# Optimization experiments

Measured on AMD Instinct MI355X. Metric: run time of the kernel, lower is better.

Reference implementation:

```python
import jax, jax.numpy as jnp
import numpy as np

# PointLSTM (CVPR'20, VIPL-SLP repo) reference.
# Layout: inputs (B, C, T, N); first OFF channels of C are point coords (x,y,z,t).
# Per timestep t: for each point, find TOPK nearest (xyz) points of frame t-1,
# gather their positions / hidden / cell states, form [feat, pos_offset, h_nbr],
# apply a shared 1x1 conv producing 4*HID gates, LSTM-gate per neighbor, then
# max-pool over the TOPK neighbors. offsets arg is accepted but unused because
# PointLSTM is constructed with offsets=False (the wrapper's default).

B, C, T, N = 4, 132, 32, 64
HID, OFF, K = 256, 4, 16


def setup_inputs() -> dict:
    key = jax.random.key(0)
    k1, k2, k3 = jax.random.split(key, 3)
    inputs = jax.random.normal(k1, (B, C, T, N), jnp.float32)
    offsets = jax.random.normal(k2, (B, OFF, T, N), jnp.float32)
    cin = C + OFF + HID  # current feat + position offset + neighbor hidden
    W = jax.random.normal(k3, (4 * HID, cin), jnp.float32) / np.sqrt(cin)
    b = jnp.zeros((4 * HID,), jnp.float32)
    return {"inputs": inputs, "offsets": offsets, "W": W, "b": b}


def _gather(x, idx):
    # x: (B, C, N), idx: (B, N, K) -> (B, C, N, K)
    return jax.vmap(lambda xb, ib: xb[:, ib])(x, idx)


def _forward(inputs, offsets, W, b):
    pos = inputs[:, :OFF]               # (B, 4, T, N)
    xs = jnp.moveaxis(inputs, 2, 0)     # (T, B, C, N)
    ps = jnp.moveaxis(pos, 2, 0)        # (T, B, 4, N)
    h0 = jnp.zeros((B, HID, N), inputs.dtype)
    c0 = jnp.zeros((B, HID, N), inputs.dtype)

    def step(carry, xt_pt):
        h, c, prev_pos = carry          # h,c: (B,HID,N); prev_pos: (B,4,N)
        xt, pt = xt_pt                  # (B,C,N), (B,4,N)
        # squared xyz distance current frame -> previous frame: (B, N, N)
        d = jnp.sum((pt[:, :3, :, None] - prev_pos[:, :3, None, :]) ** 2, axis=1)
        _, idx = jax.lax.top_k(-d, K)   # (B, N, K) nearest neighbors
        pos_g = _gather(prev_pos, idx)  # (B, 4,  N, K)
        h_g = _gather(h, idx)           # (B, HID, N, K)
        c_g = _gather(c, idx)           # (B, HID, N, K)
        off = pos_g - pt[:, :, :, None]                      # position offsets
        xk = jnp.broadcast_to(xt[:, :, :, None], (B, C, N, K))
        comb = jnp.concatenate([xk, off, h_g], axis=1)       # (B, C+4+HID, N, K)
        gates = jnp.einsum('gc,bcnk->bgnk', W, comb) + b[None, :, None, None]
        i, f, o, g = jnp.split(gates, 4, axis=1)
        c_k = jax.nn.sigmoid(f) * c_g + jax.nn.sigmoid(i) * jnp.tanh(g)
        h_k = jax.nn.sigmoid(o) * jnp.tanh(c_k)
        h_new = jnp.max(h_k, axis=-1)   # AdaptiveMaxPool2d((None,1)) over K
        c_new = jnp.max(c_k, axis=-1)
        return (h_new, c_new, pt), (h_new, idx)

    # t=0 groups against its own frame with zero hidden state (repo behavior)
    _, (hs, idxs) = jax.lax.scan(step, (h0, c0, ps[0]), (xs, ps))
    out = jnp.moveaxis(hs, 0, 2)                         # (B, HID, T, N)
    inds = jnp.moveaxis(idxs, 0, 1).astype(jnp.int32)    # (B, T, N, K)
    return out, inds


def reference(inputs, offsets, W, b):
    # Matches TestPointLSTM.forward: (output[0][0].squeeze(-1), output[2])
    return _forward(inputs, offsets, W, b)
```

## Files before the change

kernel.cpp:

```cpp
#include <hip/hip_runtime.h>
#include <math.h>

#define BB 4
#define CC 132
#define TT 32
#define NN 64
#define HIDD 256
#define G4 1024
#define CIN 392
#define KK 16
#define HOFF 136

typedef __attribute__((ext_vector_type(8))) short bf16x8;
typedef __attribute__((ext_vector_type(4))) float f32x4;

__device__ __forceinline__ float frcp(float x) { return __builtin_amdgcn_rcpf(x); }
__device__ __forceinline__ float fsigm(float x) { return frcp(1.0f + __expf(-x)); }
__device__ __forceinline__ float ftanh(float x) {
    float e = __expf(2.0f * x);
    return 1.0f - 2.0f * frcp(e + 1.0f);
}
__device__ __forceinline__ unsigned short f2bf(float x) {
    union { float f; unsigned u; } v; v.f = x;
    unsigned r = v.u + 0x7fffu + ((v.u >> 16) & 1u);
    return (unsigned short)(r >> 16);
}

__global__ __launch_bounds__(256) void ktrans2(const float* __restrict__ W,
                                               const float* __restrict__ bias,
                                               unsigned short* __restrict__ WXf,
                                               unsigned short* __restrict__ WHf,
                                               unsigned short* __restrict__ WposA,
                                               float* __restrict__ biasP) {
    int gt = blockIdx.x;
    int tid = threadIdx.x;
    __shared__ float Wl[16][CIN];
    for (int row = 0; row < 16; ++row) {
        int orig = (row & 3) * 256 + gt * 4 + (row >> 2);
        for (int c = tid; c < CIN; c += 256)
            Wl[row][c] = W[(size_t)orig * CIN + c];
    }
    __syncthreads();
    for (int f = tid; f < 320; f += 256) {
        int ks = f >> 6, l = f & 63;
        bf16x8 v;
        #pragma unroll
        for (int j = 0; j < 8; ++j) {
            int c = ks * 32 + (l >> 4) * 8 + j;
            float w = (c < CC) ? Wl[l & 15][c] : ((c < HOFF) ? -Wl[l & 15][c] : 0.0f);
            v[j] = (short)f2bf(w);
        }
        *(bf16x8*)&WXf[((size_t)(gt * 5 + ks)) * 512 + l * 8] = v;
    }
    for (int f = tid; f < 512; f += 256) {
        int ks = f >> 6, l = f & 63;
        bf16x8 v;
        #pragma unroll
        for (int j = 0; j < 8; ++j) {
            int c = HOFF + ks * 32 + (l >> 4) * 8 + j;
            v[j] = (short)f2bf(Wl[l & 15][c]);
        }
        *(bf16x8*)&WHf[((size_t)(gt * 8 + ks)) * 512 + l * 8] = v;
    }
    if (tid < 64) {
        bf16x8 v;
        #pragma unroll
        for (int e = 0; e < 8; ++e) {
            int c = (tid >> 4) * 8 + e;
            v[e] = (c < 4) ? (short)f2bf(Wl[tid & 15][CC + c]) : (short)0;
        }
        *(bf16x8*)&WposA[(size_t)gt * 512 + tid * 8] = v;
    }
    if (tid < 16)
        biasP[gt * 16 + tid] = bias[(tid & 3) * 256 + gt * 4 + (tid >> 2)];
}

__global__ __launch_bounds__(256) void kprep(const float* __restrict__ in,
                                             int* __restrict__ idxw,
                                             float* __restrict__ outI,
                                             unsigned short* __restrict__ xf,
                                             unsigned short* __restrict__ posAf) {
    int t = blockIdx.x >> 2, b = blockIdx.x & 3;
    int tid = threadIdx.x;
    int tprev = t ? t - 1 : 0;

    __shared__ unsigned short X[64][160];
    {
        int n = tid & 63, cg = tid >> 6;
        for (int c = cg; c < 160; c += 4) {
            float v = 0.0f;
            if (c < CC)        v = in[(((size_t)b * CC + c) * TT + t) * NN + n];
            else if (c < HOFF) v = in[(((size_t)b * CC + (c - CC)) * TT + t) * NN + n];
            X[n][c] = f2bf(v);
        }
        __syncthreads();
        for (int i = 0; i < 5; ++i) {
            int f = i * 256 + tid;
            int mtn = f / 320, r = f % 320;
            int ks = r >> 6, l = r & 63;
            uint4 v = *(const uint4*)&X[mtn * 16 + (l & 15)][ks * 32 + (l >> 4) * 8];
            *(uint4*)&xf[(((size_t)(blockIdx.x * 4 + mtn)) * 5 + ks) * 512 + l * 8] = v;
        }
    }
    {
        int mt = tid >> 6, l = tid & 63;
        bf16x8 v;
        #pragma unroll
        for (int e = 0; e < 8; ++e) {
            int c = (l >> 4) * 8 + e;
            float p = (c < 4) ? in[(((size_t)b * CC + c) * TT + tprev) * NN + mt * 16 + (l & 15)] : 0.0f;
            v[e] = (short)f2bf(p);
        }
        *(bf16x8*)&posAf[(((size_t)(t * BB + b)) * 4 + mt) * 512 + l * 8] = v;
    }
    {
        int lane = tid & 63, w = tid >> 6;
        const float* base = in + (size_t)b * CC * TT * NN;
        float p0 = base[(0 * TT + tprev) * NN + lane];
        float p1 = base[(1 * TT + tprev) * NN + lane];
        float p2 = base[(2 * TT + tprev) * NN + lane];
        float q0 = base[(0 * TT + t) * NN + lane];
        float q1 = base[(1 * TT + t) * NN + lane];
        float q2 = base[(2 * TT + t) * NN + lane];
        for (int nn = 0; nn < 16; ++nn) {
            int n = w * 16 + nn;
            float a0 = __shfl(q0, n), a1 = __shfl(q1, n), a2 = __shfl(q2, n);
            float dx = a0 - p0, dy = a1 - p1, dz = a2 - p2;
            float s01 = __fadd_rn(__fmul_rn(dx, dx), __fmul_rn(dy, dy));
            float d = __fadd_rn(s01, __fmul_rn(dz, dz));
            unsigned long long key =
                ((unsigned long long)__float_as_uint(d) << 32) | (unsigned)lane;
            #pragma unroll
            for (int k = 2; k <= 64; k <<= 1) {
                #pragma unroll
                for (int j = k >> 1; j > 0; j >>= 1) {
                    unsigned long long other = __shfl_xor(key, j);
                    bool up = (lane & k) == 0;
                    bool upper = (lane & j) != 0;
                    bool keepMax = up ? upper : !upper;
                    unsigned long long mn = key < other ? key : other;
                    unsigned long long mx = key < other ? other : key;
                    key = keepMax ? mx : mn;
                }
            }
            if (lane < KK) {
                int m = (int)(key & 0xffffffffu);
                idxw[((t * BB + b) * NN + n) * KK + lane] = m;
                outI[((b * TT + t) * NN + n) * KK + lane] = (float)m;
            }
        }
    }
}

__global__ __launch_bounds__(256) void kxa3(const unsigned short* __restrict__ xf,
                                            const unsigned short* __restrict__ WXf,
                                            const float* __restrict__ biasP,
                                            float* __restrict__ XA) {
    int gq = blockIdx.x & 3, tb = blockIdx.x >> 2;
    int w = threadIdx.x >> 6, l = threadIdx.x & 63;
    int gbase = gq * 16 + w * 4;
    f32x4 acc[4][4];
    #pragma unroll
    for (int a = 0; a < 4; ++a)
        #pragma unroll
        for (int g = 0; g < 4; ++g) acc[a][g] = (f32x4){0.f, 0.f, 0.f, 0.f};
    #pragma unroll
    for (int ks = 0; ks < 5; ++ks) {
        bf16x8 af[4], bfr[4];
        #pragma unroll
        for (int m = 0; m < 4; ++m)
            af[m] = *(const bf16x8*)&xf[(((size_t)(tb * 4 + m)) * 5 + ks) * 512 + l * 8];
        #pragma unroll
        for (int g = 0; g < 4; ++g)
            bfr[g] = *(const bf16x8*)&WXf[((size_t)((gbase + g) * 5 + ks)) * 512 + l * 8];
        #pragma unroll
        for (int m = 0; m < 4; ++m)
            #pragma unroll
            for (int g = 0; g < 4; ++g)
                acc[m][g] = __builtin_amdgcn_mfma_f32_16x16x32_bf16(af[m], bfr[g], acc[m][g], 0, 0, 0);
    }
    int rb = tb * 64;
    #pragma unroll
    for (int g = 0; g < 4; ++g) {
        int gcol = (gbase + g) * 16 + (l & 15);
        float bv = biasP[gcol];
        #pragma unroll
        for (int m = 0; m < 4; ++m)
            #pragma unroll
            for (int r = 0; r < 4; ++r) {
                int row = rb + m * 16 + (l >> 4) * 4 + r;
                XA[(size_t)row * G4 + gcol] = acc[m][g][r] + bv;
            }
    }
}

__global__ __launch_bounds__(512) void kstep(const float* __restrict__ XA,
                                             const unsigned short* __restrict__ WHf,
                                             const unsigned short* __restrict__ WposA,
                                             const unsigned short* __restrict__ posAf,
                                             const unsigned short* __restrict__ hr,
                                             unsigned short* __restrict__ hw,
                                             const int* __restrict__ idxw,
                                             const float* __restrict__ cp,
                                             float* __restrict__ cn,
                                             float* __restrict__ out, int t) {
    int bid = blockIdx.x;
    int b = bid & 3, q = (bid >> 2) & 15, nh = bid >> 6;
    int tid = threadIdx.x;
    __shared__ float LDSG[64][68];
    __shared__ float cmbH[256], cmbC[256];

    int kh = tid >> 8, p = tid & 255;
    int nl = p >> 4, jl = p & 15;
    int n = nh * 16 + nl;
    int jg = q * 16 + jl;

    const int* irow = &idxw[((size_t)(t * BB + b) * NN + n) * KK + kh * 8];
    int4 mi0 = *(const int4*)irow;
    int4 mi1 = *(const int4*)(irow + 4);
    const float4 xav = *(const float4*)&XA[((size_t)(t * BB + b) * NN + n) * G4 + jg * 4];

    {
        int wv = tid >> 6, l = tid & 63;
        int mt = wv & 3, gh = wv >> 2;
        bf16x8 bf[8];
        if (t > 0) {
            #pragma unroll
            for (int ks = 0; ks < 8; ++ks)
                bf[ks] = *(const bf16x8*)&hr[(((size_t)(b * 4 + mt)) * 8 + ks) * 512 + l * 8];
        }
        bf16x8 bp = *(const bf16x8*)&posAf[(((size_t)(t * BB + b)) * 4 + mt) * 512 + l * 8];
        #pragma unroll
        for (int gg = 0; gg < 2; ++gg) {
            int gtl = gh * 2 + gg;
            int gt = q * 4 + gtl;
            f32x4 a0 = {0.f, 0.f, 0.f, 0.f};
            f32x4 a1 = {0.f, 0.f, 0.f, 0.f};
            if (t > 0) {
                #pragma unroll
                for (int ks = 0; ks < 8; ks += 2) {
                    bf16x8 af0 = *(const bf16x8*)&WHf[(((size_t)gt) * 8 + ks) * 512 + l * 8];
                    bf16x8 af1 = *(const bf16x8*)&WHf[(((size_t)gt) * 8 + ks + 1) * 512 + l * 8];
                    a0 = __builtin_amdgcn_mfma_f32_16x16x32_bf16(af0, bf[ks], a0, 0, 0, 0);
                    a1 = __builtin_amdgcn_mfma_f32_16x16x32_bf16(af1, bf[ks + 1], a1, 0, 0, 0);
                }
            }
            bf16x8 ap = *(const bf16x8*)&WposA[(size_t)gt * 512 + l * 8];
            a0 = __builtin_amdgcn_mfma_f32_16x16x32_bf16(ap, bp, a0, 0, 0, 0);
            a0[0] += a1[0]; a0[1] += a1[1]; a0[2] += a1[2]; a0[3] += a1[3];
            *(f32x4*)&LDSG[mt * 16 + (l & 15)][gtl * 16 + (l >> 4) * 4] = a0;
        }
    }

    float cgv[8] = {0.f, 0.f, 0.f, 0.f, 0.f, 0.f, 0.f, 0.f};
    if (t > 0) {
        const float* cb = cp + (size_t)b * NN * HIDD + jg;
        cgv[0] = cb[(size_t)mi0.x * HIDD];
        cgv[1] = cb[(size_t)mi0.y * HIDD];
        cgv[2] = cb[(size_t)mi0.z * HIDD];
        cgv[3] = cb[(size_t)mi0.w * HIDD];
        cgv[4] = cb[(size_t)mi1.x * HIDD];
        cgv[5] = cb[(size_t)mi1.y * HIDD];
        cgv[6] = cb[(size_t)mi1.z * HIDD];
        cgv[7] = cb[(size_t)mi1.w * HIDD];
    }
    __syncthreads();

    {
        int ms[8] = {mi0.x, mi0.y, mi0.z, mi0.w, mi1.x, mi1.y, mi1.z, mi1.w};
        float hmax = -INFINITY, cmax = -INFINITY;
        #pragma unroll
        for (int kk = 0; kk < 8; ++kk) {
            int m = ms[kk];
            f32x4 g = *(const f32x4*)&LDSG[m][jl * 4];
            float gi = xav.x + g[0];
            float gf = xav.y + g[1];
            float go = xav.z + g[2];
            float gg = xav.w + g[3];
            float ck = fsigm(gf) * cgv[kk] + fsigm(gi) * ftanh(gg);
            float hk = fsigm(go) * ftanh(ck);
            hmax = fmaxf(hmax, hk);
            cmax = fmaxf(cmax, ck);
        }
        if (kh == 1) { cmbH[p] = hmax; cmbC[p] = cmax; }
        __syncthreads();
        if (kh == 0) {
            hmax = fmaxf(hmax, cmbH[p]);
            cmax = fmaxf(cmax, cmbC[p]);
            cn[((size_t)b * NN + n) * HIDD + jg] = cmax;
            out[((size_t)(b * HIDD + jg) * TT + t) * NN + n] = hmax;
            hw[(((size_t)(b * 4 + (n >> 4))) * 8 + (jg >> 5)) * 512 +
               (((jg >> 3) & 3) * 16 + (n & 15)) * 8 + (jg & 7)] = f2bf(hmax);
        }
    }
}

extern "C" void kernel_launch(void* const* d_in, const int* in_sizes, int n_in,
                              void* d_out, int out_size, void* d_ws, size_t ws_size,
                              hipStream_t stream) {
    const float* in   = (const float*)d_in[0];
    const float* W    = (const float*)d_in[2];
    const float* bias = (const float*)d_in[3];
    float* out  = (float*)d_out;
    float* outI = out + (size_t)BB * HIDD * TT * NN;

    float* ws     = (float*)d_ws;
    float* XA     = ws;
    float* biasP  = XA + (size_t)TT * BB * NN * G4;
    float* c0     = biasP + G4;
    float* c1     = c0 + (size_t)BB * NN * HIDD;
    unsigned short* WXf   = (unsigned short*)(c1 + (size_t)BB * NN * HIDD);
    unsigned short* WHf   = WXf + (size_t)64 * 5 * 512;
    unsigned short* WposA = WHf + (size_t)64 * 8 * 512;
    unsigned short* xf    = WposA + (size_t)64 * 512;
    unsigned short* hb0   = xf + (size_t)128 * 4 * 5 * 512;
    unsigned short* hb1   = hb0 + (size_t)BB * NN * HIDD;
    unsigned short* posAf = hb1 + (size_t)BB * NN * HIDD;
    int* idxw = (int*)(posAf + (size_t)TT * BB * 4 * 512);

    ktrans2<<<64, 256, 0, stream>>>(W, bias, WXf, WHf, WposA, biasP);
    kprep<<<128, 256, 0, stream>>>(in, idxw, outI, xf, posAf);
    kxa3<<<512, 256, 0, stream>>>(xf, WXf, biasP, XA);

    for (int t = 0; t < TT; ++t) {
        float* cpb = (t & 1) ? c0 : c1;
        float* cnb = (t & 1) ? c1 : c0;
        unsigned short* hrd = (t & 1) ? hb0 : hb1;
        unsigned short* hwr = (t & 1) ? hb1 : hb0;
        kstep<<<256, 512, 0, stream>>>(XA, WHf, WposA, posAf, hrd, hwr,
                                       idxw, cpb, cnb, out, t);
    }
}
```

Baseline: 308.0 us.

## Fuse setup kernels and compute input-gate projection inside each step kernel

Merges the weight-transpose, input-prep and top-k kernels into a single setup launch, splitting top-k across more blocks. The separate precomputed input projection (a large fp32 XA buffer written once and read every step) is removed. Each step kernel now computes its 16x64 slice of the input gate projection with extra MFMAs into shared memory. This cuts launches and XA global traffic, but adds matrix work on the serial per-step critical path.

```diff
diff --git a/kernel.cpp b/kernel.cpp
--- a/kernel.cpp
+++ b/kernel.cpp
@@ -26,94 +26,106 @@
     return (unsigned short)(r >> 16);
 }
 
-__global__ __launch_bounds__(256) void ktrans2(const float* __restrict__ W,
-                                               const float* __restrict__ bias,
-                                               unsigned short* __restrict__ WXf,
-                                               unsigned short* __restrict__ WHf,
-                                               unsigned short* __restrict__ WposA,
-                                               float* __restrict__ biasP) {
-    int gt = blockIdx.x;
-    int tid = threadIdx.x;
-    __shared__ float Wl[16][CIN];
-    for (int row = 0; row < 16; ++row) {
-        int orig = (row & 3) * 256 + gt * 4 + (row >> 2);
-        for (int c = tid; c < CIN; c += 256)
-            Wl[row][c] = W[(size_t)orig * CIN + c];
-    }
-    __syncthreads();
-    for (int f = tid; f < 320; f += 256) {
-        int ks = f >> 6, l = f & 63;
-        bf16x8 v;
-        #pragma unroll
-        for (int j = 0; j < 8; ++j) {
-            int c = ks * 32 + (l >> 4) * 8 + j;
-            float w = (c < CC) ? Wl[l & 15][c] : ((c < HOFF) ? -Wl[l & 15][c] : 0.0f);
-            v[j] = (short)f2bf(w);
-        }
-        *(bf16x8*)&WXf[((size_t)(gt * 5 + ks)) * 512 + l * 8] = v;
-    }
-    for (int f = tid; f < 512; f += 256) {
-        int ks = f >> 6, l = f & 63;
-        bf16x8 v;
-        #pragma unroll
-        for (int j = 0; j < 8; ++j) {
-            int c = HOFF + ks * 32 + (l >> 4) * 8 + j;
-            v[j] = (short)f2bf(Wl[l & 15][c]);
-        }
-        *(bf16x8*)&WHf[((size_t)(gt * 8 + ks)) * 512 + l * 8] = v;
-    }
-    if (tid < 64) {
-        bf16x8 v;
-        #pragma unroll
-        for (int e = 0; e < 8; ++e) {
-            int c = (tid >> 4) * 8 + e;
-            v[e] = (c < 4) ? (short)f2bf(Wl[tid & 15][CC + c]) : (short)0;
-        }
-        *(bf16x8*)&WposA[(size_t)gt * 512 + tid * 8] = v;
-    }
-    if (tid < 16)
-        biasP[gt * 16 + tid] = bias[(tid & 3) * 256 + gt * 4 + (tid >> 2)];
-}
-
-__global__ __launch_bounds__(256) void kprep(const float* __restrict__ in,
-                                             int* __restrict__ idxw,
-                                             float* __restrict__ outI,
-                                             unsigned short* __restrict__ xf,
-                                             unsigned short* __restrict__ posAf) {
-    int t = blockIdx.x >> 2, b = blockIdx.x & 3;
-    int tid = threadIdx.x;
-    int tprev = t ? t - 1 : 0;
-
-    __shared__ unsigned short X[64][160];
-    {
-        int n = tid & 63, cg = tid >> 6;
-        for (int c = cg; c < 160; c += 4) {
-            float v = 0.0f;
-            if (c < CC)        v = in[(((size_t)b * CC + c) * TT + t) * NN + n];
-            else if (c < HOFF) v = in[(((size_t)b * CC + (c - CC)) * TT + t) * NN + n];
-            X[n][c] = f2bf(v);
+__global__ __launch_bounds__(256) void ksetup(const float* __restrict__ in,
+                                              const float* __restrict__ W,
+                                              const float* __restrict__ bias,
+                                              unsigned short* __restrict__ WXf,
+                                              unsigned short* __restrict__ WHf,
+                                              unsigned short* __restrict__ WposA,
+                                              float* __restrict__ biasP,
+                                              unsigned short* __restrict__ xf,
+                                              unsigned short* __restrict__ posAf,
+                                              int* __restrict__ idxw,
+                                              float* __restrict__ outI) {
+    __shared__ __align__(16) char smem[16 * CIN * 4];
+    int bid = blockIdx.x, tid = threadIdx.x;
+
+    if (bid < 64) {
+        int gt = bid;
+        float (*Wl)[CIN] = (float(*)[CIN])smem;
+        for (int row = 0; row < 16; ++row) {
+            int orig = (row & 3) * 256 + gt * 4 + (row >> 2);
+            for (int c = tid; c < CIN; c += 256)
+                Wl[row][c] = W[(size_t)orig * CIN + c];
         }
         __syncthreads();
-        for (int i = 0; i < 5; ++i) {
-            int f = i * 256 + tid;
-            int mtn = f / 320, r = f % 320;
-            int ks = r >> 6, l = r & 63;
-            uint4 v = *(const uint4*)&X[mtn * 16 + (l & 15)][ks * 32 + (l >> 4) * 8];
-            *(uint4*)&xf[(((size_t)(blockIdx.x * 4 + mtn)) * 5 + ks) * 512 + l * 8] = v;
-        }
-    }
-    {
-        int mt = tid >> 6, l = tid & 63;
-        bf16x8 v;
-        #pragma unroll
-        for (int e = 0; e < 8; ++e) {
-            int c = (l >> 4) * 8 + e;
-            float p = (c < 4) ? in[(((size_t)b * CC + c) * TT + tprev) * NN + mt * 16 + (l & 15)] : 0.0f;
-            v[e] = (short)f2bf(p);
-        }
-        *(bf16x8*)&posAf[(((size_t)(t * BB + b)) * 4 + mt) * 512 + l * 8] = v;
-    }
-    {
+        for (int f = tid; f < 320; f += 256) {
+            int ks = f >> 6, l = f & 63;
+            bf16x8 v;
+            #pragma unroll
+            for (int j = 0; j < 8; ++j) {
+                int c = ks * 32 + (l >> 4) * 8 + j;
+                float w = (c < CC) ? Wl[l & 15][c] : ((c < HOFF) ? -Wl[l & 15][c] : 0.0f);
+                v[j] = (short)f2bf(w);
+            }
+            *(bf16x8*)&WXf[((size_t)(gt * 5 + ks)) * 512 + l * 8] = v;
+        }
+        for (int f = tid; f < 512; f += 256) {
+            int ks = f >> 6, l = f & 63;
+            bf16x8 v;
+            #pragma unroll
+            for (int j = 0; j < 8; ++j) {
+                int c = HOFF + ks * 32 + (l >> 4) * 8 + j;
+                v[j] = (short)f2bf(Wl[l & 15][c]);
+            }
+            *(bf16x8*)&WHf[((size_t)(gt * 8 + ks)) * 512 + l * 8] = v;
+        }
+        if (tid < 64) {
+            bf16x8 v;
+            #pragma unroll
+            for (int e = 0; e < 8; ++e) {
+                int c = (tid >> 4) * 8 + e;
+                v[e] = (c < 4) ? (short)f2bf(Wl[tid & 15][CC + c]) : (short)0;
+            }
+            *(bf16x8*)&WposA[(size_t)gt * 512 + tid * 8] = v;
+        }
+        if (tid < 16)
+            biasP[gt * 16 + tid] = bias[(tid & 3) * 256 + gt * 4 + (tid >> 2)];
+    } else if (bid < 192) {
+        int tb = bid - 64;
+        int t = tb >> 2, b = tb & 3;
+        int tprev = t ? t - 1 : 0;
+        unsigned short (*X)[168] = (unsigned short(*)[168])smem;
+        {
+            int n = tid & 63, cg = tid >> 6;
+            #pragma unroll
+            for (int i = 0; i < 10; ++i) {
+                int c = cg * 4 + i * 16;
+                short4 s;
+                #pragma unroll
+                for (int j = 0; j < 4; ++j) {
+                    int cc = c + j;
+                    float v = 0.0f;
+                    if (cc < CC)        v = in[(((size_t)b * CC + cc) * TT + t) * NN + n];
+                    else if (cc < HOFF) v = in[(((size_t)b * CC + (cc - CC)) * TT + t) * NN + n];
+                    ((unsigned short*)&s)[j] = f2bf(v);
+                }
+                *(short4*)&X[n][c] = s;
+            }
+            __syncthreads();
+            for (int i = 0; i < 5; ++i) {
+                int f = i * 256 + tid;
+                int mtn = f / 320, r = f % 320;
+                int ks = r >> 6, l = r & 63;
+                uint4 v = *(const uint4*)&X[mtn * 16 + (l & 15)][ks * 32 + (l >> 4) * 8];
+                *(uint4*)&xf[(((size_t)(tb * 4 + mtn)) * 5 + ks) * 512 + l * 8] = v;
+            }
+        }
+        {
+            int mt = tid >> 6, l = tid & 63;
+            bf16x8 v;
+            #pragma unroll
+            for (int e = 0; e < 8; ++e) {
+                int c = (l >> 4) * 8 + e;
+                float p = (c < 4) ? in[(((size_t)b * CC + c) * TT + tprev) * NN + mt * 16 + (l & 15)] : 0.0f;
+                v[e] = (short)f2bf(p);
+            }
+            *(bf16x8*)&posAf[(((size_t)(t * BB + b)) * 4 + mt) * 512 + l * 8] = v;
+        }
+    } else {
+        int idx2 = bid - 192;
+        int tb = idx2 >> 2, qr = idx2 & 3;
+        int t = tb >> 2, b = tb & 3, tprev = t ? t - 1 : 0;
         int lane = tid & 63, w = tid >> 6;
         const float* base = in + (size_t)b * CC * TT * NN;
         float p0 = base[(0 * TT + tprev) * NN + lane];
@@ -122,8 +134,8 @@
         float q0 = base[(0 * TT + t) * NN + lane];
         float q1 = base[(1 * TT + t) * NN + lane];
         float q2 = base[(2 * TT + t) * NN + lane];
-        for (int nn = 0; nn < 16; ++nn) {
-            int n = w * 16 + nn;
+        for (int nn = 0; nn < 4; ++nn) {
+            int n = qr * 16 + w * 4 + nn;
             float a0 = __shfl(q0, n), a1 = __shfl(q1, n), a2 = __shfl(q2, n);
             float dx = a0 - p0, dy = a1 - p1, dz = a2 - p2;
             float s01 = __fadd_rn(__fmul_rn(dx, dx), __fmul_rn(dy, dy));
@@ -152,52 +164,12 @@
     }
 }
 
-__global__ __launch_bounds__(256) void kxa3(const unsigned short* __restrict__ xf,
-                                            const unsigned short* __restrict__ WXf,
-                                            const float* __restrict__ biasP,
-                                            float* __restrict__ XA) {
-    int gq = blockIdx.x & 3, tb = blockIdx.x >> 2;
-    int w = threadIdx.x >> 6, l = threadIdx.x & 63;
-    int gbase = gq * 16 + w * 4;
-    f32x4 acc[4][4];
-    #pragma unroll
-    for (int a = 0; a < 4; ++a)
-        #pragma unroll
-        for (int g = 0; g < 4; ++g) acc[a][g] = (f32x4){0.f, 0.f, 0.f, 0.f};
-    #pragma unroll
-    for (int ks = 0; ks < 5; ++ks) {
-        bf16x8 af[4], bfr[4];
-        #pragma unroll
-        for (int m = 0; m < 4; ++m)
-            af[m] = *(const bf16x8*)&xf[(((size_t)(tb * 4 + m)) * 5 + ks) * 512 + l * 8];
-        #pragma unroll
-        for (int g = 0; g < 4; ++g)
-            bfr[g] = *(const bf16x8*)&WXf[((size_t)((gbase + g) * 5 + ks)) * 512 + l * 8];
-        #pragma unroll
-        for (int m = 0; m < 4; ++m)
-            #pragma unroll
-            for (int g = 0; g < 4; ++g)
-                acc[m][g] = __builtin_amdgcn_mfma_f32_16x16x32_bf16(af[m], bfr[g], acc[m][g], 0, 0, 0);
-    }
-    int rb = tb * 64;
-    #pragma unroll
-    for (int g = 0; g < 4; ++g) {
-        int gcol = (gbase + g) * 16 + (l & 15);
-        float bv = biasP[gcol];
-        #pragma unroll
-        for (int m = 0; m < 4; ++m)
-            #pragma unroll
-            for (int r = 0; r < 4; ++r) {
-                int row = rb + m * 16 + (l >> 4) * 4 + r;
-                XA[(size_t)row * G4 + gcol] = acc[m][g][r] + bv;
-            }
-    }
-}
-
-__global__ __launch_bounds__(512) void kstep(const float* __restrict__ XA,
-                                             const unsigned short* __restrict__ WHf,
+__global__ __launch_bounds__(512) void kstep(const unsigned short* __restrict__ WHf,
                                              const unsigned short* __restrict__ WposA,
+                                             const unsigned short* __restrict__ WXf,
+                                             const unsigned short* __restrict__ xf,
                                              const unsigned short* __restrict__ posAf,
+                                             const float* __restrict__ biasP,
                                              const unsigned short* __restrict__ hr,
                                              unsigned short* __restrict__ hw,
                                              const int* __restrict__ idxw,
@@ -208,6 +180,7 @@
     int b = bid & 3, q = (bid >> 2) & 15, nh = bid >> 6;
     int tid = threadIdx.x;
     __shared__ float LDSG[64][68];
+    __shared__ float XAL[16][68];
     __shared__ float cmbH[256], cmbC[256];
 
     int kh = tid >> 8, p = tid & 255;
@@ -218,7 +191,6 @@
     const int* irow = &idxw[((size_t)(t * BB + b) * NN + n) * KK + kh * 8];
     int4 mi0 = *(const int4*)irow;
     int4 mi1 = *(const int4*)(irow + 4);
-    const float4 xav = *(const float4*)&XA[((size_t)(t * BB + b) * NN + n) * G4 + jg * 4];
 
     {
         int wv = tid >> 6, l = tid & 63;
@@ -250,6 +222,19 @@
             a0[0] += a1[0]; a0[1] += a1[1]; a0[2] += a1[2]; a0[3] += a1[3];
             *(f32x4*)&LDSG[mt * 16 + (l & 15)][gtl * 16 + (l >> 4) * 4] = a0;
         }
+        if (gh == 1) {
+            int gtl = mt, gt = q * 4 + gtl;
+            f32x4 a = {0.f, 0.f, 0.f, 0.f};
+            #pragma unroll
+            for (int ks = 0; ks < 5; ++ks) {
+                bf16x8 aw = *(const bf16x8*)&WXf[((size_t)(gt * 5 + ks)) * 512 + l * 8];
+                bf16x8 bx = *(const bf16x8*)&xf[((((size_t)(t * BB + b)) * 4 + nh) * 5 + ks) * 512 + l * 8];
+                a = __builtin_amdgcn_mfma_f32_16x16x32_bf16(aw, bx, a, 0, 0, 0);
+            }
+            f32x4 bv = *(const f32x4*)&biasP[gt * 16 + (l >> 4) * 4];
+            a[0] += bv[0]; a[1] += bv[1]; a[2] += bv[2]; a[3] += bv[3];
+            *(f32x4*)&XAL[l & 15][gtl * 16 + (l >> 4) * 4] = a;
+        }
     }
 
     float cgv[8] = {0.f, 0.f, 0.f, 0.f, 0.f, 0.f, 0.f, 0.f};
@@ -267,16 +252,17 @@
     __syncthreads();
 
     {
+        const f32x4 xav = *(const f32x4*)&XAL[nl][jl * 4];
         int ms[8] = {mi0.x, mi0.y, mi0.z, mi0.w, mi1.x, mi1.y, mi1.z, mi1.w};
         float hmax = -INFINITY, cmax = -INFINITY;
         #pragma unroll
         for (int kk = 0; kk < 8; ++kk) {
             int m = ms[kk];
             f32x4 g = *(const f32x4*)&LDSG[m][jl * 4];
-            float gi = xav.x + g[0];
-            float gf = xav.y + g[1];
-            float go = xav.z + g[2];
-            float gg = xav.w + g[3];
+            float gi = xav[0] + g[0];
+            float gf = xav[1] + g[1];
+            float go = xav[2] + g[2];
+            float gg = xav[3] + g[3];
             float ck = fsigm(gf) * cgv[kk] + fsigm(gi) * ftanh(gg);
             float hk = fsigm(go) * ftanh(ck);
             hmax = fmaxf(hmax, hk);
@@ -305,8 +291,7 @@
     float* outI = out + (size_t)BB * HIDD * TT * NN;
 
     float* ws     = (float*)d_ws;
-    float* XA     = ws;
-    float* biasP  = XA + (size_t)TT * BB * NN * G4;
+    float* biasP  = ws;
     float* c0     = biasP + G4;
     float* c1     = c0 + (size_t)BB * NN * HIDD;
     unsigned short* WXf   = (unsigned short*)(c1 + (size_t)BB * NN * HIDD);
@@ -318,16 +303,15 @@
     unsigned short* posAf = hb1 + (size_t)BB * NN * HIDD;
     int* idxw = (int*)(posAf + (size_t)TT * BB * 4 * 512);
 
-    ktrans2<<<64, 256, 0, stream>>>(W, bias, WXf, WHf, WposA, biasP);
-    kprep<<<128, 256, 0, stream>>>(in, idxw, outI, xf, posAf);
-    kxa3<<<512, 256, 0, stream>>>(xf, WXf, biasP, XA);
+    ksetup<<<704, 256, 0, stream>>>(in, W, bias, WXf, WHf, WposA, biasP,
+                                    xf, posAf, idxw, outI);
 
     for (int t = 0; t < TT; ++t) {
         float* cpb = (t & 1) ? c0 : c1;
         float* cnb = (t & 1) ? c1 : c0;
         unsigned short* hrd = (t & 1) ? hb0 : hb1;
         unsigned short* hwr = (t & 1) ? hb1 : hb0;
-        kstep<<<256, 512, 0, stream>>>(XA, WHf, WposA, posAf, hrd, hwr,
-                                       idxw, cpb, cnb, out, t);
-    }
-}
+        kstep<<<256, 512, 0, stream>>>(WHf, WposA, WXf, xf, posAf, biasP,
+                                       hrd, hwr, idxw, cpb, cnb, out, t);
+    }
+}
```

Measured after the change: 270.8 us. 12.1% less time.
